# Kernel tuning notes

Hardware: AMD Instinct MI355X
Metric: run time of the kernel (lower is better)

## Reference

```python
import jax, jax.numpy as jnp
import numpy as np

B, SQ, SK, D = 8, 4096, 4096, 64


def setup_inputs() -> dict:
    key = jax.random.key(0)
    k1, k2, k3 = jax.random.split(key, 3)
    x1 = jax.random.normal(k1, (B, SQ, D), dtype=jnp.float32)   # queries
    x2 = jax.random.normal(k2, (B, SK, D), dtype=jnp.float32)   # keys
    x3 = jax.random.normal(k3, (B, SK, D), dtype=jnp.float32)   # values
    x4 = 0                                                      # dropout p (static, 0 => deterministic)
    x5 = jnp.ones((1,), dtype=jnp.float32)                      # scale divisor
    return {"x1": x1, "x2": x2, "x3": x3, "x4": x4, "x5": x5}


def reference(x1, x2, x3, x4, x5):
    # scores: [B, Sq, Sk]
    scores = jnp.einsum("bqd,bkd->bqk", x1, x2) / x5
    attn = jax.nn.softmax(scores, axis=-1)
    p = float(x4)  # static python scalar
    if p > 0.0:
        mask = jax.random.bernoulli(jax.random.key(42), 1.0 - p, attn.shape)
        attn = attn * mask.astype(attn.dtype) / (1.0 - p)
    # out: [B, Sq, D]
    return jnp.einsum("bqk,bkd->bqd", attn, x3)
```

## Files before the change

### kernel.cpp

```cpp
#include <hip/hip_runtime.h>


typedef _Float16 f16x8 __attribute__((ext_vector_type(8)));
typedef _Float16 f16x4 __attribute__((ext_vector_type(4)));
typedef __fp16   h16x2 __attribute__((ext_vector_type(2)));
typedef float    f32x4 __attribute__((ext_vector_type(4)));
typedef float    f32x16 __attribute__((ext_vector_type(16)));

constexpr int kB  = 8;
constexpr int kSQ = 4096;
constexpr int kSK = 4096;
constexpr int kD  = 64;
constexpr int KSPLIT = 4;
constexpr int SKH = kSK / KSPLIT;
constexpr int BQ  = 256;
constexpr int MT  = 2;
constexpr int BK  = 64;
constexpr size_t APART = (size_t)kB * kSQ * kD;
constexpr float kLog2e = 1.44269504088896340736f;
constexpr float kDeferThr = 11.5f;

static __device__ __forceinline__ f16x4 pack4(float a, float b, float c, float d) {
    h16x2 p0 = __builtin_amdgcn_cvt_pkrtz(a, b);
    h16x2 p1 = __builtin_amdgcn_cvt_pkrtz(c, d);
    f16x4 r;
    r[0] = (_Float16)p0[0]; r[1] = (_Float16)p0[1];
    r[2] = (_Float16)p1[0]; r[3] = (_Float16)p1[1];
    return r;
}
static __device__ __forceinline__ f16x8 pack8(const float4& a, const float4& c) {
    f16x4 lo = pack4(a.x, a.y, a.z, a.w);
    f16x4 hi = pack4(c.x, c.y, c.z, c.w);
    f16x8 f;
    f[0] = lo[0]; f[1] = lo[1]; f[2] = lo[2]; f[3] = lo[3];
    f[4] = hi[0]; f[5] = hi[1]; f[6] = hi[2]; f[7] = hi[3];
    return f;
}
static __device__ __forceinline__ unsigned pkrtz_u(float a, float b) {
    union { h16x2 h; unsigned u; } cv;
    cv.h = __builtin_amdgcn_cvt_pkrtz(a, b);
    return cv.u;
}

typedef const __attribute__((address_space(1))) unsigned int* gu32p;
typedef __attribute__((address_space(3))) unsigned int* lu32p;
static __device__ __forceinline__ void gload_lds16(const void* g, void* l) {
    __builtin_amdgcn_global_load_lds((gu32p)g, (lu32p)l, 16, 0, 0);
}

#define PA_SLICE(dst, sv, rb) do {                                          \
    unsigned c0 = pkrtz_u((sv)[(rb)+0], (sv)[(rb)+1]);                      \
    unsigned c1 = pkrtz_u((sv)[(rb)+2], (sv)[(rb)+3]);                      \
    unsigned c2 = pkrtz_u((sv)[(rb)+4], (sv)[(rb)+5]);                      \
    unsigned c3 = pkrtz_u((sv)[(rb)+6], (sv)[(rb)+7]);                      \
    auto r02 = __builtin_amdgcn_permlane32_swap(c0, c2, false, false);      \
    auto r13 = __builtin_amdgcn_permlane32_swap(c1, c3, false, false);      \
    union { unsigned u[4]; f16x8 v; } _r;                                   \
    _r.u[0] = r02[0]; _r.u[1] = r13[0]; _r.u[2] = r02[1]; _r.u[3] = r13[1]; \
    dst = _r.v;                                                             \
} while (0)

__global__ __launch_bounds__(256, 2)
void fattn_prepass(const float* __restrict__ Kg,
                   const float* __restrict__ Vg,
                   _Float16* __restrict__ Kh,
                   _Float16* __restrict__ Vt)
{
    __shared__ _Float16 tr[kD][BK];

    const int tid = threadIdx.x;
    const int kt  = blockIdx.x;
    const int b   = blockIdx.y;

    const int k = tid >> 2;
    const int p = tid & 3;
    const int gk = kt * BK + k;

    {
        const float* src = Kg + ((size_t)b * kSK + gk) * kD + p * 16;
        const float4 a0 = *(const float4*)(src + 0);
        const float4 a1 = *(const float4*)(src + 4);
        const float4 a2 = *(const float4*)(src + 8);
        const float4 a3 = *(const float4*)(src + 12);
        _Float16* dst = Kh + ((size_t)b * kSK + gk) * kD;
        const int fb0 = 2 * p, fb1 = 2 * p + 1;
        *(f16x8*)&dst[(fb0 ^ (gk & 7)) * 8] = pack8(a0, a1);
        *(f16x8*)&dst[(fb1 ^ (gk & 7)) * 8] = pack8(a2, a3);
    }
    {
        const float* src = Vg + ((size_t)b * kSK + gk) * kD + p * 16;
        const float4 a0 = *(const float4*)(src + 0);
        const float4 a1 = *(const float4*)(src + 4);
        const float4 a2 = *(const float4*)(src + 8);
        const float4 a3 = *(const float4*)(src + 12);
        const float v[16] = {a0.x,a0.y,a0.z,a0.w, a1.x,a1.y,a1.z,a1.w,
                             a2.x,a2.y,a2.z,a2.w, a3.x,a3.y,a3.z,a3.w};
#pragma unroll
        for (int j = 0; j < 16; ++j)
            tr[p * 16 + j][k] = (_Float16)v[j];
    }
    __syncthreads();
    {
        const int f  = tid >> 2;
        const int p2 = tid & 3;
        const f16x8 b0 = *(const f16x8*)&tr[f][p2 * 16 + 0];
        const f16x8 b1 = *(const f16x8*)&tr[f][p2 * 16 + 8];
        _Float16* dst = Vt + (((size_t)b * 64 + kt) * kD + f) * BK;
        const int kb0 = 2 * p2, kb1 = 2 * p2 + 1;
        *(f16x8*)&dst[(kb0 ^ (f & 7)) * 8] = b0;
        *(f16x8*)&dst[(kb1 ^ (f & 7)) * 8] = b1;
    }
}

__global__ __launch_bounds__(256, 2)
void fattn_partial(const float* __restrict__ Qg,
                   const _Float16* __restrict__ Kh,
                   const _Float16* __restrict__ Vt,
                   const float* __restrict__ sdiv,
                   _Float16* __restrict__ Ap,
                   float2* __restrict__ MLp)
{
    __shared__ __align__(16) _Float16 sK[2][BK * kD];
    __shared__ __align__(16) _Float16 sV[2][kD * BK];

    const int tid  = threadIdx.x;
    const int w    = tid >> 6;
    const int lane = tid & 63;
    const int l31  = lane & 31;
    const int hi   = lane >> 5;

    const int flat = blockIdx.x;
    const int c    = flat & 31;
    const int qi   = flat >> 5;
    const int b    = c >> 2;
    const int ks   = c & 3;
    const int qb   = qi * BQ;

    const float qscale = kLog2e / sdiv[0];

    const float* Qb = Qg + ((size_t)b * kSQ + qb) * kD;
    const _Float16* Khb = Kh + ((size_t)b * kSK + (size_t)ks * SKH) * kD;
    const _Float16* Vtb = Vt + (((size_t)b * 64 + (size_t)ks * (SKH / BK)) * kD) * BK;

    f16x8 qf[MT][4];
#pragma unroll
    for (int mt = 0; mt < MT; ++mt) {
        const float* qrow = Qb + (size_t)(w * 64 + mt * 32 + l31) * kD;
#pragma unroll
        for (int ds = 0; ds < 4; ++ds) {
            const float4 a  = *(const float4*)(qrow + ds * 16 + hi * 8);
            const float4 cc = *(const float4*)(qrow + ds * 16 + hi * 8 + 4);
            float4 as = make_float4(a.x * qscale, a.y * qscale, a.z * qscale, a.w * qscale);
            float4 cs = make_float4(cc.x * qscale, cc.y * qscale, cc.z * qscale, cc.w * qscale);
            qf[mt][ds] = pack8(as, cs);
        }
    }

    int offA[4];
#pragma unroll
    for (int i = 0; i < 4; ++i)
        offA[i] = l31 * 64 + (((2 * i + hi) ^ (l31 & 7)) * 8);

    auto stage = [&](int kt, int buf) {
        const char* gk = (const char*)(Khb + (size_t)kt * BK * kD) + w * 2048 + lane * 16;
        const char* gv = (const char*)(Vtb + (size_t)kt * kD * BK) + w * 2048 + lane * 16;
        char* lk = (char*)&sK[buf][0] + w * 2048;
        char* lv = (char*)&sV[buf][0] + w * 2048;
        gload_lds16(gk,        lk);
        gload_lds16(gk + 1024, lk + 1024);
        gload_lds16(gv,        lv);
        gload_lds16(gv + 1024, lv + 1024);
    };

    f32x16 oL[MT], oH[MT];
    float m_i[MT], ll[MT];
#pragma unroll
    for (int mt = 0; mt < MT; ++mt) {
        m_i[mt] = -1e30f; ll[mt] = 0.0f;
#pragma unroll
        for (int r = 0; r < 16; ++r) { oL[mt][r] = 0.0f; oH[mt][r] = 0.0f; }
    }

    stage(0, 0);
    __syncthreads();

    const int nIter = SKH / BK;
    for (int kt = 0; kt < nIter; ++kt) {
        const int buf = kt & 1;
        if (kt + 1 < nIter) stage(kt + 1, buf ^ 1);

        f16x8 vf[4][2];
#pragma unroll
        for (int s = 0; s < 4; ++s) {
            vf[s][0] = *(const f16x8*)&sV[buf][offA[s]];
            vf[s][1] = *(const f16x8*)&sV[buf][offA[s] + 2048];
        }

#pragma unroll
        for (int mt = 0; mt < MT; ++mt) {
            f32x16 s0, s1;
#pragma unroll
            for (int r = 0; r < 16; ++r) { s0[r] = 0.0f; s1[r] = 0.0f; }
#pragma unroll
            for (int ds = 0; ds < 4; ++ds) {
                const f16x8 kf0 = *(const f16x8*)&sK[buf][offA[ds]];
                const f16x8 kf1 = *(const f16x8*)&sK[buf][offA[ds] + 2048];
                s0 = __builtin_amdgcn_mfma_f32_32x32x16_f16(kf0, qf[mt][ds], s0, 0, 0, 0);
                s1 = __builtin_amdgcn_mfma_f32_32x32x16_f16(kf1, qf[mt][ds], s1, 0, 0, 0);
            }

            float t[16];
#pragma unroll
            for (int r = 0; r < 16; ++r) t[r] = fmaxf(s0[r], s1[r]);
#pragma unroll
            for (int r = 0; r < 8; ++r)  t[r] = fmaxf(t[r], t[r + 8]);
#pragma unroll
            for (int r = 0; r < 4; ++r)  t[r] = fmaxf(t[r], t[r + 4]);
            float rm = fmaxf(fmaxf(t[0], t[1]), fmaxf(t[2], t[3]));
            rm = fmaxf(rm, __shfl_xor(rm, 32, 64));

            if (!__all(rm <= m_i[mt] + kDeferThr)) {
                const float mnew  = fmaxf(m_i[mt], rm);
                const float alpha = __builtin_amdgcn_exp2f(m_i[mt] - mnew);
                ll[mt] *= alpha;
#pragma unroll
                for (int r = 0; r < 16; ++r) { oL[mt][r] *= alpha; oH[mt][r] *= alpha; }
                m_i[mt] = mnew;
            }

#pragma unroll
            for (int r = 0; r < 16; ++r) {
                s0[r] = __builtin_amdgcn_exp2f(s0[r] - m_i[mt]);
                s1[r] = __builtin_amdgcn_exp2f(s1[r] - m_i[mt]);
            }

            {
                float a0 = 0.f, a1 = 0.f, a2 = 0.f, a3 = 0.f;
#pragma unroll
                for (int r = 0; r < 16; r += 4) {
                    a0 += s0[r]; a1 += s0[r + 1]; a2 += s0[r + 2]; a3 += s0[r + 3];
                    a0 += s1[r]; a1 += s1[r + 1]; a2 += s1[r + 2]; a3 += s1[r + 3];
                }
                ll[mt] += (a0 + a1) + (a2 + a3);
            }

            f16x8 pa[4];
            PA_SLICE(pa[0], s0, 0);
            PA_SLICE(pa[1], s0, 8);
            PA_SLICE(pa[2], s1, 0);
            PA_SLICE(pa[3], s1, 8);

#pragma unroll
            for (int s = 0; s < 4; ++s) {
                oL[mt] = __builtin_amdgcn_mfma_f32_32x32x16_f16(vf[s][0], pa[s], oL[mt], 0, 0, 0);
                oH[mt] = __builtin_amdgcn_mfma_f32_32x32x16_f16(vf[s][1], pa[s], oH[mt], 0, 0, 0);
            }
        }

        __syncthreads();
    }

    _Float16* Ab = Ap + (size_t)ks * APART + ((size_t)b * kSQ + qb) * kD;
    float2* MLb = MLp + (size_t)ks * kB * kSQ + (size_t)b * kSQ + qb;
#pragma unroll
    for (int mt = 0; mt < MT; ++mt) {
        const int q = w * 64 + mt * 32 + l31;
        const float lf = ll[mt] + __shfl_xor(ll[mt], 32, 64);
        const float inv = 1.0f / lf;
        _Float16* arow = &Ab[(size_t)q * kD];
#pragma unroll
        for (int g = 0; g < 4; ++g) {
            *(f16x4*)&arow[g * 8 + hi * 4] =
                pack4(oL[mt][4 * g] * inv, oL[mt][4 * g + 1] * inv,
                      oL[mt][4 * g + 2] * inv, oL[mt][4 * g + 3] * inv);
            *(f16x4*)&arow[32 + g * 8 + hi * 4] =
                pack4(oH[mt][4 * g] * inv, oH[mt][4 * g + 1] * inv,
                      oH[mt][4 * g + 2] * inv, oH[mt][4 * g + 3] * inv);
        }
        if (hi == 0) MLb[q] = make_float2(m_i[mt], lf);
    }
}

__global__ __launch_bounds__(256)
void fattn_combine(const _Float16* __restrict__ Ap,
                   const float2* __restrict__ MLp,
                   float* __restrict__ Og)
{
    const int idx = blockIdx.x * 256 + threadIdx.x;
    const int r = idx >> 4;
    const int c = (idx & 15) * 4;

    float m = -1e30f;
    float2 ml[KSPLIT];
#pragma unroll
    for (int s = 0; s < KSPLIT; ++s) {
        ml[s] = MLp[(size_t)s * kB * kSQ + r];
        m = fmaxf(m, ml[s].x);
    }
    float acc[4] = {0.f, 0.f, 0.f, 0.f};
    float lsum = 0.f;
#pragma unroll
    for (int s = 0; s < KSPLIT; ++s) {
        const float wgt = __builtin_amdgcn_exp2f(ml[s].x - m) * ml[s].y;
        lsum += wgt;
        const f16x4 a = *(const f16x4*)&Ap[(size_t)s * APART + (size_t)r * kD + c];
#pragma unroll
        for (int j = 0; j < 4; ++j) acc[j] += wgt * (float)a[j];
    }
    const float inv = 1.0f / lsum;
    float4 res = make_float4(acc[0] * inv, acc[1] * inv, acc[2] * inv, acc[3] * inv);
    *(float4*)&Og[(size_t)r * kD + c] = res;
}

extern "C" void kernel_launch(void* const* d_in, const int* in_sizes, int n_in,
                              void* d_out, int out_size, void* d_ws, size_t ws_size,
                              hipStream_t stream) {
    const float* Q    = (const float*)d_in[0];
    const float* K    = (const float*)d_in[1];
    const float* V    = (const float*)d_in[2];
    const float* sdiv = (const float*)d_in[4];
    float* O = (float*)d_out;

    _Float16* Kh  = (_Float16*)d_ws;
    _Float16* Vt  = Kh + (size_t)kB * kSK * kD;
    _Float16* Ap  = Vt + (size_t)kB * kSK * kD;
    float2*   MLp = (float2*)(Ap + (size_t)KSPLIT * APART);

    fattn_prepass<<<dim3(kSK / BK, kB), dim3(256), 0, stream>>>(K, V, Kh, Vt);
    fattn_partial<<<dim3((kSQ / BQ) * kB * KSPLIT), dim3(256), 0, stream>>>(Q, Kh, Vt, sdiv, Ap, MLp);
    fattn_combine<<<dim3(kB * kSQ * kD / (256 * 4)), dim3(256), 0, stream>>>(Ap, MLp, O);
}
```

Baseline: 135.0 us.

## Hoist QK MFMAs across tiles, compute row sums via MFMA, add setprio

Loads the K fragments once per tile and issues all QK^T MFMAs for both m-tiles up front, wrapping the MFMA blocks in s_setprio so matrix work overlaps the softmax of the other tile. The per-row sum of P, previously a VALU reduction plus a cross-half shuffle, is now an extra MFMA against a vector of ones. The row-max cross-half shuffle becomes a permlane32_swap. The trade-off is more accumulator registers (two sets of score tiles plus an extra accumulator per m-tile), which could lower occupancy, and row sums built from the fp16-rounded P values.

```diff
diff --git a/kernel.cpp b/kernel.cpp
--- a/kernel.cpp
+++ b/kernel.cpp
@@ -41,6 +41,13 @@
     cv.h = __builtin_amdgcn_cvt_pkrtz(a, b);
     return cv.u;
 }
+static __device__ __forceinline__ float xhalf_max(float x) {
+    union { float f; unsigned u; } uv; uv.f = x;
+    auto pr = __builtin_amdgcn_permlane32_swap(uv.u, uv.u, false, false);
+    union { unsigned u; float f; } r0, r1;
+    r0.u = pr[0]; r1.u = pr[1];
+    return fmaxf(r0.f, r1.f);
+}
 
 typedef const __attribute__((address_space(1))) unsigned int* gu32p;
 typedef __attribute__((address_space(3))) unsigned int* lu32p;
@@ -156,6 +163,10 @@
         }
     }
 
+    f16x8 ones;
+#pragma unroll
+    for (int j = 0; j < 8; ++j) ones[j] = (_Float16)1.0f;
+
     int offA[4];
 #pragma unroll
     for (int i = 0; i < 4; ++i)
@@ -173,12 +184,14 @@
     };
 
     f32x16 oL[MT], oH[MT];
-    float m_i[MT], ll[MT];
+    f32x16 ol[MT];
+    float m_i[MT];
 #pragma unroll
     for (int mt = 0; mt < MT; ++mt) {
-        m_i[mt] = -1e30f; ll[mt] = 0.0f;
-#pragma unroll
-        for (int r = 0; r < 16; ++r) { oL[mt][r] = 0.0f; oH[mt][r] = 0.0f; }
+        m_i[mt] = -1e30f;
+        ol[mt][0] = 0.0f;
+#pragma unroll
+        for (int r = 0; r < 16; ++r) { oL[mt][r] = 0.0f; oH[mt][r] = 0.0f; ol[mt][r] = 0.0f; }
     }
 
     stage(0, 0);
@@ -189,6 +202,29 @@
         const int buf = kt & 1;
         if (kt + 1 < nIter) stage(kt + 1, buf ^ 1);
 
+        f16x8 kf0[4], kf1[4];
+#pragma unroll
+        for (int ds = 0; ds < 4; ++ds) {
+            kf0[ds] = *(const f16x8*)&sK[buf][offA[ds]];
+            kf1[ds] = *(const f16x8*)&sK[buf][offA[ds] + 2048];
+        }
+
+        f32x16 s0[MT], s1[MT];
+#pragma unroll
+        for (int mt = 0; mt < MT; ++mt)
+#pragma unroll
+            for (int r = 0; r < 16; ++r) { s0[mt][r] = 0.0f; s1[mt][r] = 0.0f; }
+
+        __builtin_amdgcn_s_setprio(1);
+#pragma unroll
+        for (int ds = 0; ds < 4; ++ds)
+#pragma unroll
+            for (int mt = 0; mt < MT; ++mt) {
+                s0[mt] = __builtin_amdgcn_mfma_f32_32x32x16_f16(kf0[ds], qf[mt][ds], s0[mt], 0, 0, 0);
+                s1[mt] = __builtin_amdgcn_mfma_f32_32x32x16_f16(kf1[ds], qf[mt][ds], s1[mt], 0, 0, 0);
+            }
+        __builtin_amdgcn_s_setprio(0);
+
         f16x8 vf[4][2];
 #pragma unroll
         for (int s = 0; s < 4; ++s) {
@@ -198,31 +234,20 @@
 
 #pragma unroll
         for (int mt = 0; mt < MT; ++mt) {
-            f32x16 s0, s1;
-#pragma unroll
-            for (int r = 0; r < 16; ++r) { s0[r] = 0.0f; s1[r] = 0.0f; }
-#pragma unroll
-            for (int ds = 0; ds < 4; ++ds) {
-                const f16x8 kf0 = *(const f16x8*)&sK[buf][offA[ds]];
-                const f16x8 kf1 = *(const f16x8*)&sK[buf][offA[ds] + 2048];
-                s0 = __builtin_amdgcn_mfma_f32_32x32x16_f16(kf0, qf[mt][ds], s0, 0, 0, 0);
-                s1 = __builtin_amdgcn_mfma_f32_32x32x16_f16(kf1, qf[mt][ds], s1, 0, 0, 0);
-            }
-
             float t[16];
 #pragma unroll
-            for (int r = 0; r < 16; ++r) t[r] = fmaxf(s0[r], s1[r]);
+            for (int r = 0; r < 16; ++r) t[r] = fmaxf(s0[mt][r], s1[mt][r]);
 #pragma unroll
             for (int r = 0; r < 8; ++r)  t[r] = fmaxf(t[r], t[r + 8]);
 #pragma unroll
             for (int r = 0; r < 4; ++r)  t[r] = fmaxf(t[r], t[r + 4]);
             float rm = fmaxf(fmaxf(t[0], t[1]), fmaxf(t[2], t[3]));
-            rm = fmaxf(rm, __shfl_xor(rm, 32, 64));
+            rm = xhalf_max(rm);
 
             if (!__all(rm <= m_i[mt] + kDeferThr)) {
                 const float mnew  = fmaxf(m_i[mt], rm);
                 const float alpha = __builtin_amdgcn_exp2f(m_i[mt] - mnew);
-                ll[mt] *= alpha;
+                ol[mt][0] *= alpha;
 #pragma unroll
                 for (int r = 0; r < 16; ++r) { oL[mt][r] *= alpha; oH[mt][r] *= alpha; }
                 m_i[mt] = mnew;
@@ -230,31 +255,24 @@
 
 #pragma unroll
             for (int r = 0; r < 16; ++r) {
-                s0[r] = __builtin_amdgcn_exp2f(s0[r] - m_i[mt]);
-                s1[r] = __builtin_amdgcn_exp2f(s1[r] - m_i[mt]);
+                s0[mt][r] = __builtin_amdgcn_exp2f(s0[mt][r] - m_i[mt]);
+                s1[mt][r] = __builtin_amdgcn_exp2f(s1[mt][r] - m_i[mt]);
             }
 
-            {
-                float a0 = 0.f, a1 = 0.f, a2 = 0.f, a3 = 0.f;
-#pragma unroll
-                for (int r = 0; r < 16; r += 4) {
-                    a0 += s0[r]; a1 += s0[r + 1]; a2 += s0[r + 2]; a3 += s0[r + 3];
-                    a0 += s1[r]; a1 += s1[r + 1]; a2 += s1[r + 2]; a3 += s1[r + 3];
-                }
-                ll[mt] += (a0 + a1) + (a2 + a3);
-            }
-
             f16x8 pa[4];
-            PA_SLICE(pa[0], s0, 0);
-            PA_SLICE(pa[1], s0, 8);
-            PA_SLICE(pa[2], s1, 0);
-            PA_SLICE(pa[3], s1, 8);
-
+            PA_SLICE(pa[0], s0[mt], 0);
+            PA_SLICE(pa[1], s0[mt], 8);
+            PA_SLICE(pa[2], s1[mt], 0);
+            PA_SLICE(pa[3], s1[mt], 8);
+
+            __builtin_amdgcn_s_setprio(1);
 #pragma unroll
             for (int s = 0; s < 4; ++s) {
                 oL[mt] = __builtin_amdgcn_mfma_f32_32x32x16_f16(vf[s][0], pa[s], oL[mt], 0, 0, 0);
                 oH[mt] = __builtin_amdgcn_mfma_f32_32x32x16_f16(vf[s][1], pa[s], oH[mt], 0, 0, 0);
+                ol[mt] = __builtin_amdgcn_mfma_f32_32x32x16_f16(ones,     pa[s], ol[mt], 0, 0, 0);
             }
+            __builtin_amdgcn_s_setprio(0);
         }
 
         __syncthreads();
@@ -265,7 +283,7 @@
 #pragma unroll
     for (int mt = 0; mt < MT; ++mt) {
         const int q = w * 64 + mt * 32 + l31;
-        const float lf = ll[mt] + __shfl_xor(ll[mt], 32, 64);
+        const float lf = ol[mt][0];
         const float inv = 1.0f / lf;
         _Float16* arow = &Ab[(size_t)q * kD];
 #pragma unroll
```

Result: no change. 133.8 us (-0.9%).
